# Optimization experiments

Hardware: AMD Instinct MI355X
Metric: run time of the kernel (lower is better)

Reference implementation:

```python
import jax, jax.numpy as jnp
import numpy as np

B, L, D = 16, 2048, 128
NEG = -1.0e9


def setup_inputs() -> dict:
    key = jax.random.key(0)
    kq, kk, kv, km = jax.random.split(key, 4)
    Q = jax.random.normal(kq, (B, L, D), dtype=jnp.float32)
    K = jax.random.normal(kk, (B, L, D), dtype=jnp.float32)
    V = jax.random.normal(kv, (B, L, D), dtype=jnp.float32)
    scale = jnp.float32(1.0 / np.sqrt(D))
    # original code masks rows where (mask + 1) == 0, i.e. mask == -1
    mask = jnp.where(jax.random.uniform(km, (B, L)) < 0.1, -1, 0).astype(jnp.int32)
    return {"Q": Q, "K": K, "V": V, "scale": scale, "mask": mask}


def reference(Q, K, V, scale, mask):
    # attention = Q @ K^T * scale  -> [B, Lq, Lk]
    att = jnp.einsum("bqd,bkd->bqk", Q, K) * scale
    # mask[b, i] broadcast over the key dim j (row-wise masking, as in the
    # original unsqueeze(-1).expand pattern with square attention)
    row_masked = (mask + 1) == 0  # [B, L]
    att = jnp.where(row_masked[:, :, None], NEG, att)
    att = jax.nn.softmax(att, axis=-1)
    context = jnp.einsum("bqk,bkd->bqd", att, V)
    return context
```

## Files before the change

### kernel.cpp

```cpp
#include <hip/hip_runtime.h>


#define NB 16
#define LL 2048
#define DD 128
#define LOG2E 1.44269504f
#define NM (-9.0f * 1.44269504f)

typedef __attribute__((ext_vector_type(8))) short short8;
typedef __attribute__((ext_vector_type(16))) float f32x16;

__device__ __forceinline__ float wexp2(float x) {
  float r; asm("v_exp_f32 %0, %1" : "=v"(r) : "v"(x)); return r;
}
__device__ __forceinline__ unsigned cvtpk(float lo, float hi) {
  unsigned r; asm("v_cvt_pk_bf16_f32 %0, %1, %2" : "=v"(r) : "v"(lo), "v"(hi)); return r;
}
__device__ __forceinline__ void gll16(const void* g, const void* l) {
  __builtin_amdgcn_global_load_lds(
      (const __attribute__((address_space(1))) unsigned*)g,
      (__attribute__((address_space(3))) unsigned*)l, 16, 0, 0);
}

__global__ void prep_kv(const float* __restrict__ K, const float* __restrict__ V,
                        short* __restrict__ Kb, short* __restrict__ Vt) {
  __shared__ short lds[64 * 130];
  int bid = blockIdx.x;
  int t = threadIdx.x;
  if (bid < 2048) {
    int g = bid * 256 + t;
    const float4* kp = (const float4*)K + (size_t)g * 2;
    float4 a = kp[0], c = kp[1];
    ((uint4*)Kb)[g] = make_uint4(cvtpk(a.x, a.y), cvtpk(a.z, a.w),
                                 cvtpk(c.x, c.y), cvtpk(c.z, c.w));
    return;
  }
  int vb = bid - 2048;
  int b = vb >> 5;
  int t0 = (vb & 31) * 64;
  #pragma unroll
  for (int i = 0; i < 8; ++i) {
    int c = t + i * 256;
    int kv = c >> 5, ds = (c & 31) * 4;
    float4 v = *(const float4*)(V + ((size_t)(b * LL + t0 + kv) * DD + ds));
    unsigned* dst = (unsigned*)(&lds[kv * 130 + ds]);
    dst[0] = cvtpk(v.x, v.y);
    dst[1] = cvtpk(v.z, v.w);
  }
  __syncthreads();
  int d = t >> 1, hf = t & 1;
  unsigned dw[16];
  #pragma unroll
  for (int i = 0; i < 16; ++i) {
    int kv = hf * 32 + i * 2;
    unsigned lo16 = (unsigned short)lds[kv * 130 + d];
    unsigned hi16 = (unsigned short)lds[(kv + 1) * 130 + d];
    dw[i] = lo16 | (hi16 << 16);
  }
  short* orow = Vt + (size_t)(b * DD + d) * LL + t0 + hf * 32;
  #pragma unroll
  for (int i = 0; i < 4; ++i)
    ((uint4*)orow)[i] = make_uint4(dw[4 * i], dw[4 * i + 1], dw[4 * i + 2], dw[4 * i + 3]);
}

__global__ __launch_bounds__(512, 2) void attn_main(
    const float* __restrict__ Q, const float* __restrict__ scl,
    const int* __restrict__ mask, const short* __restrict__ Kb,
    const short* __restrict__ Vt, float* __restrict__ Out) {
  __shared__ __align__(16) char smem[99840];
  const int tid = threadIdx.x;
  const int w = tid >> 6, l = tid & 63, lo = l & 31, hi = l >> 5;
  const int qg = w & 3, kvh = w >> 2;

  int lg = (blockIdx.x & 7) * 32 + (blockIdx.x >> 3);
  int b = lg >> 4;
  int q0 = (lg & 15) * 128 + qg * 32;

  int qrow = b * LL + q0 + lo;
  float msc = (mask[qrow] == -1) ? 0.f : scl[0];
  short8 qf[8];
  {
    const float* qp = Q + (size_t)qrow * DD + hi * 8;
    #pragma unroll
    for (int dc = 0; dc < 8; ++dc) {
      float4 a = *(const float4*)(qp + dc * 16);
      float4 c = *(const float4*)(qp + dc * 16 + 4);
      union { unsigned u[4]; short8 s; } pu;
      pu.u[0] = cvtpk(a.x * msc, a.y * msc);
      pu.u[1] = cvtpk(a.z * msc, a.w * msc);
      pu.u[2] = cvtpk(c.x * msc, c.y * msc);
      pu.u[3] = cvtpk(c.z * msc, c.w * msc);
      qf[dc] = pu.s;
    }
  }

  const char* kgb = (const char*)(Kb + (size_t)b * (LL * DD));
  const char* vgb = (const char*)(Vt + (size_t)b * (LL * DD));

#define STAGE(bi_, kv0_) do { \
    char* kbuf = smem + (bi_) * 16384; \
    char* vbuf = smem + 49152 + (bi_) * 16384; \
    _Pragma("unroll") \
    for (int i = 0; i < 2; ++i) { \
      int c = w * 2 + i; \
      int kr = c * 4 + (l >> 4); \
      int kc = ((l & 15) << 4) ^ ((kr & 15) << 4); \
      gll16(kgb + (size_t)((kv0_) + kr) * 256 + kc, kbuf + c * 1024); \
      int vr = c * 8 + (l >> 3); \
      int vc = ((l & 7) << 4) ^ ((vr & 7) << 4); \
      gll16(vgb + (size_t)vr * 4096 + (size_t)(kv0_) * 2 + vc, vbuf + c * 1024); \
    } \
  } while (0)

  STAGE(0, 0);
  STAGE(1, 64);

  f32x16 oacc[4];
  #pragma unroll
  for (int dt = 0; dt < 4; ++dt)
    #pragma unroll
    for (int r = 0; r < 16; ++r) oacc[dt][r] = 0.f;
  float lsum = 0.f;

  const int swzk = (lo & 15) << 4;
  const int swzv = (lo & 7) << 4;

  int cb = 0, sb = 2;
  #pragma unroll 1
  for (int t = 0; t < 32; ++t) {
    if (t == 31) { asm volatile("s_waitcnt vmcnt(0)" ::: "memory"); }
    else         { asm volatile("s_waitcnt vmcnt(4)" ::: "memory"); }
    __builtin_amdgcn_s_barrier();
    __builtin_amdgcn_sched_barrier(0);
    if (t < 30) STAGE(sb, (t + 2) * 64);

    const char* kb = smem + cb * 16384;
    const char* vb = smem + 49152 + cb * 16384;

    f32x16 acc;
    #pragma unroll
    for (int r = 0; r < 16; ++r) acc[r] = 0.f;
    const char* krow = kb + (kvh * 32 + lo) * 256;
    #pragma unroll
    for (int dc = 0; dc < 8; ++dc) {
      short8 kf = *(const short8*)(krow + ((dc * 32 + hi * 16) ^ swzk));
      acc = __builtin_amdgcn_mfma_f32_32x32x16_bf16(kf, qf[dc], acc, 0, 0, 0);
    }
    float ps = 0.f;
    #pragma unroll
    for (int r = 0; r < 16; ++r) {
      float p = wexp2(__builtin_fmaf(acc[r], LOG2E, NM));
      acc[r] = p; ps += p;
    }
    lsum += ps;
    short8 pa[2];
    #pragma unroll
    for (int ks = 0; ks < 2; ++ks) {
      unsigned a0 = cvtpk(acc[ks * 8 + 0], acc[ks * 8 + 1]);
      unsigned b0 = cvtpk(acc[ks * 8 + 4], acc[ks * 8 + 5]);
      unsigned c0 = cvtpk(acc[ks * 8 + 2], acc[ks * 8 + 3]);
      unsigned d0 = cvtpk(acc[ks * 8 + 6], acc[ks * 8 + 7]);
      asm volatile("v_permlane32_swap_b32 %0, %1" : "+v"(a0), "+v"(b0));
      asm volatile("v_permlane32_swap_b32 %0, %1" : "+v"(c0), "+v"(d0));
      union { unsigned u[4]; short8 s; } pu;
      pu.u[0] = a0; pu.u[1] = c0; pu.u[2] = b0; pu.u[3] = d0;
      pa[ks] = pu.s;
    }
    #pragma unroll
    for (int dt = 0; dt < 4; ++dt) {
      const char* vrow = vb + (dt * 32 + lo) * 128;
      #pragma unroll
      for (int ks = 0; ks < 2; ++ks) {
        short8 vf = *(const short8*)(vrow + ((kvh * 64 + ks * 32 + hi * 16) ^ swzv));
        oacc[dt] = __builtin_amdgcn_mfma_f32_32x32x16_bf16(pa[ks], vf, oacc[dt], 0, 0, 0);
      }
    }
    cb = (cb == 2) ? 0 : cb + 1;
    sb = (sb == 2) ? 0 : sb + 1;
  }
#undef STAGE

  float* lsb = (float*)(smem + 98304);
  float* rdb = (float*)(smem + 98304 + 1024);
  __syncthreads();
  if (kvh == 1) {
    char* reg = smem + qg * 16384;
    #pragma unroll
    for (int dt = 0; dt < 4; ++dt)
      #pragma unroll
      for (int i = 0; i < 4; ++i)
        *(float4*)(reg + l * 256 + ((dt * 64 + i * 16) ^ ((l & 15) << 4))) =
            make_float4(oacc[dt][4 * i], oacc[dt][4 * i + 1],
                        oacc[dt][4 * i + 2], oacc[dt][4 * i + 3]);
    lsb[qg * 64 + l] = lsum;
  }
  __syncthreads();
  if (kvh == 0) {
    char* reg = smem + qg * 16384;
    lsum += lsb[qg * 64 + l];
    #pragma unroll
    for (int dt = 0; dt < 4; ++dt)
      #pragma unroll
      for (int i = 0; i < 4; ++i) {
        float4 p = *(const float4*)(reg + l * 256 + ((dt * 64 + i * 16) ^ ((l & 15) << 4)));
        oacc[dt][4 * i + 0] += p.x;
        oacc[dt][4 * i + 1] += p.y;
        oacc[dt][4 * i + 2] += p.z;
        oacc[dt][4 * i + 3] += p.w;
      }
    float lt = lsum + __shfl_xor(lsum, 32);
    float rd = 1.0f / lt;
    if (l < 32) rdb[qg * 32 + l] = rd;
    #pragma unroll
    for (int r = 0; r < 16; ++r) {
      int cr = (r & 3) + 8 * (r >> 2) + 4 * hi;
      float rr = rdb[qg * 32 + cr];
      float* op = Out + (size_t)(b * LL + q0 + cr) * DD + lo;
      #pragma unroll
      for (int dt = 0; dt < 4; ++dt)
        op[dt * 32] = oacc[dt][r] * rr;
    }
  }
}

extern "C" void kernel_launch(void* const* d_in, const int* in_sizes, int n_in,
                              void* d_out, int out_size, void* d_ws, size_t ws_size,
                              hipStream_t stream) {
  const float* Q = (const float*)d_in[0];
  const float* K = (const float*)d_in[1];
  const float* V = (const float*)d_in[2];
  const float* scale = (const float*)d_in[3];
  const int* mask = (const int*)d_in[4];
  float* out = (float*)d_out;

  const size_t tensor_elems = (size_t)NB * LL * DD;
  const size_t need = 2 * tensor_elems * sizeof(short);
  if (ws_size < need) return;

  short* Kbp = (short*)d_ws;
  short* Vtp = Kbp + tensor_elems;

  hipLaunchKernelGGL(prep_kv, dim3(2560), dim3(256), 0, stream, K, V, Kbp, Vtp);
  hipLaunchKernelGGL(attn_main, dim3(256), dim3(512), 0, stream, Q, scale, mask, Kbp, Vtp, out);
}
```

Before: 60.67 us.

## Enlarge KV tile to 128 rows with double buffering in attention loop

The KV tile per iteration doubles to 128 rows and the pipeline goes from triple to double buffering, halving loop iterations and barriers. Each wave now computes two independent QK MFMA chains and feeds four P fragments into the PV MFMAs, which adds instruction-level parallelism. In exchange, shared memory use rises to about 130 KB, the prefetch depth shrinks to one tile with a full vmcnt(0) wait each iteration, and per-block occupancy may fall.

```diff
diff --git a/kernel.cpp b/kernel.cpp
--- a/kernel.cpp
+++ b/kernel.cpp
@@ -67,7 +67,7 @@
     const float* __restrict__ Q, const float* __restrict__ scl,
     const int* __restrict__ mask, const short* __restrict__ Kb,
     const short* __restrict__ Vt, float* __restrict__ Out) {
-  __shared__ __align__(16) char smem[99840];
+  __shared__ __align__(16) char smem[132608];
   const int tid = threadIdx.x;
   const int w = tid >> 6, l = tid & 63, lo = l & 31, hi = l >> 5;
   const int qg = w & 3, kvh = w >> 2;
@@ -75,6 +75,24 @@
   int lg = (blockIdx.x & 7) * 32 + (blockIdx.x >> 3);
   int b = lg >> 4;
   int q0 = (lg & 15) * 128 + qg * 32;
+
+  const char* kgb = (const char*)(Kb + (size_t)b * (LL * DD));
+  const char* vgb = (const char*)(Vt + (size_t)b * (LL * DD));
+
+#define STAGE(bi_, kv0_) do { \
+    char* kbuf = smem + (bi_) * 32768; \
+    char* vbuf = smem + 65536 + (bi_) * 32768; \
+    _Pragma("unroll") \
+    for (int i = 0; i < 4; ++i) { \
+      int c = tid + i * 512; \
+      int kr = c >> 4; \
+      int kc = ((c & 15) << 4) ^ ((kr & 15) << 4); \
+      gll16(kgb + (size_t)((kv0_) + kr) * 256 + kc, kbuf + c * 16); \
+      gll16(vgb + (size_t)kr * 4096 + (size_t)(kv0_) * 2 + kc, vbuf + c * 16); \
+    } \
+  } while (0)
+
+  STAGE(0, 0);
 
   int qrow = b * LL + q0 + lo;
   float msc = (mask[qrow] == -1) ? 0.f : scl[0];
@@ -94,27 +112,6 @@
     }
   }
 
-  const char* kgb = (const char*)(Kb + (size_t)b * (LL * DD));
-  const char* vgb = (const char*)(Vt + (size_t)b * (LL * DD));
-
-#define STAGE(bi_, kv0_) do { \
-    char* kbuf = smem + (bi_) * 16384; \
-    char* vbuf = smem + 49152 + (bi_) * 16384; \
-    _Pragma("unroll") \
-    for (int i = 0; i < 2; ++i) { \
-      int c = w * 2 + i; \
-      int kr = c * 4 + (l >> 4); \
-      int kc = ((l & 15) << 4) ^ ((kr & 15) << 4); \
-      gll16(kgb + (size_t)((kv0_) + kr) * 256 + kc, kbuf + c * 1024); \
-      int vr = c * 8 + (l >> 3); \
-      int vc = ((l & 7) << 4) ^ ((vr & 7) << 4); \
-      gll16(vgb + (size_t)vr * 4096 + (size_t)(kv0_) * 2 + vc, vbuf + c * 1024); \
-    } \
-  } while (0)
-
-  STAGE(0, 0);
-  STAGE(1, 64);
-
   f32x16 oacc[4];
   #pragma unroll
   for (int dt = 0; dt < 4; ++dt)
@@ -122,66 +119,72 @@
     for (int r = 0; r < 16; ++r) oacc[dt][r] = 0.f;
   float lsum = 0.f;
 
-  const int swzk = (lo & 15) << 4;
-  const int swzv = (lo & 7) << 4;
-
-  int cb = 0, sb = 2;
+  const int swz = (lo & 15) << 4;
+
+  int cur = 0;
   #pragma unroll 1
-  for (int t = 0; t < 32; ++t) {
-    if (t == 31) { asm volatile("s_waitcnt vmcnt(0)" ::: "memory"); }
-    else         { asm volatile("s_waitcnt vmcnt(4)" ::: "memory"); }
+  for (int t = 0; t < 16; ++t) {
+    asm volatile("s_waitcnt vmcnt(0)" ::: "memory");
     __builtin_amdgcn_s_barrier();
     __builtin_amdgcn_sched_barrier(0);
-    if (t < 30) STAGE(sb, (t + 2) * 64);
-
-    const char* kb = smem + cb * 16384;
-    const char* vb = smem + 49152 + cb * 16384;
-
-    f32x16 acc;
-    #pragma unroll
-    for (int r = 0; r < 16; ++r) acc[r] = 0.f;
-    const char* krow = kb + (kvh * 32 + lo) * 256;
+    if (t < 15) STAGE(cur ^ 1, (t + 1) * 128);
+
+    const char* kb = smem + cur * 32768;
+    const char* vb = smem + 65536 + cur * 32768;
+
+    f32x16 accA, accB;
+    #pragma unroll
+    for (int r = 0; r < 16; ++r) { accA[r] = 0.f; accB[r] = 0.f; }
+    const char* krow0 = kb + (kvh * 64 + lo) * 256;
+    const char* krow1 = kb + (kvh * 64 + 32 + lo) * 256;
     #pragma unroll
     for (int dc = 0; dc < 8; ++dc) {
-      short8 kf = *(const short8*)(krow + ((dc * 32 + hi * 16) ^ swzk));
-      acc = __builtin_amdgcn_mfma_f32_32x32x16_bf16(kf, qf[dc], acc, 0, 0, 0);
+      int kcol = (dc * 32 + hi * 16) ^ swz;
+      short8 kfA = *(const short8*)(krow0 + kcol);
+      short8 kfB = *(const short8*)(krow1 + kcol);
+      accA = __builtin_amdgcn_mfma_f32_32x32x16_bf16(kfA, qf[dc], accA, 0, 0, 0);
+      accB = __builtin_amdgcn_mfma_f32_32x32x16_bf16(kfB, qf[dc], accB, 0, 0, 0);
     }
     float ps = 0.f;
     #pragma unroll
     for (int r = 0; r < 16; ++r) {
-      float p = wexp2(__builtin_fmaf(acc[r], LOG2E, NM));
-      acc[r] = p; ps += p;
+      float pA = wexp2(__builtin_fmaf(accA[r], LOG2E, NM));
+      float pB = wexp2(__builtin_fmaf(accB[r], LOG2E, NM));
+      accA[r] = pA; accB[r] = pB; ps += pA + pB;
     }
     lsum += ps;
-    short8 pa[2];
-    #pragma unroll
-    for (int ks = 0; ks < 2; ++ks) {
-      unsigned a0 = cvtpk(acc[ks * 8 + 0], acc[ks * 8 + 1]);
-      unsigned b0 = cvtpk(acc[ks * 8 + 4], acc[ks * 8 + 5]);
-      unsigned c0 = cvtpk(acc[ks * 8 + 2], acc[ks * 8 + 3]);
-      unsigned d0 = cvtpk(acc[ks * 8 + 6], acc[ks * 8 + 7]);
-      asm volatile("v_permlane32_swap_b32 %0, %1" : "+v"(a0), "+v"(b0));
-      asm volatile("v_permlane32_swap_b32 %0, %1" : "+v"(c0), "+v"(d0));
-      union { unsigned u[4]; short8 s; } pu;
-      pu.u[0] = a0; pu.u[1] = c0; pu.u[2] = b0; pu.u[3] = d0;
-      pa[ks] = pu.s;
+    short8 pa[4];
+    #pragma unroll
+    for (int bk = 0; bk < 2; ++bk) {
+      const f32x16& ac = bk ? accB : accA;
+      #pragma unroll
+      for (int ks = 0; ks < 2; ++ks) {
+        unsigned a0 = cvtpk(ac[ks * 8 + 0], ac[ks * 8 + 1]);
+        unsigned b0 = cvtpk(ac[ks * 8 + 4], ac[ks * 8 + 5]);
+        unsigned c0 = cvtpk(ac[ks * 8 + 2], ac[ks * 8 + 3]);
+        unsigned d0 = cvtpk(ac[ks * 8 + 6], ac[ks * 8 + 7]);
+        asm volatile("v_permlane32_swap_b32 %0, %1" : "+v"(a0), "+v"(b0));
+        asm volatile("v_permlane32_swap_b32 %0, %1" : "+v"(c0), "+v"(d0));
+        union { unsigned u[4]; short8 s; } pu;
+        pu.u[0] = a0; pu.u[1] = c0; pu.u[2] = b0; pu.u[3] = d0;
+        pa[bk * 2 + ks] = pu.s;
+      }
     }
     #pragma unroll
     for (int dt = 0; dt < 4; ++dt) {
-      const char* vrow = vb + (dt * 32 + lo) * 128;
-      #pragma unroll
-      for (int ks = 0; ks < 2; ++ks) {
-        short8 vf = *(const short8*)(vrow + ((kvh * 64 + ks * 32 + hi * 16) ^ swzv));
-        oacc[dt] = __builtin_amdgcn_mfma_f32_32x32x16_bf16(pa[ks], vf, oacc[dt], 0, 0, 0);
+      const char* vrow = vb + (dt * 32 + lo) * 256;
+      #pragma unroll
+      for (int j = 0; j < 4; ++j) {
+        short8 vf = *(const short8*)(vrow + ((kvh * 128 + j * 32 + hi * 16) ^ swz));
+        oacc[dt] = __builtin_amdgcn_mfma_f32_32x32x16_bf16(pa[j], vf, oacc[dt], 0, 0, 0);
       }
     }
-    cb = (cb == 2) ? 0 : cb + 1;
-    sb = (sb == 2) ? 0 : sb + 1;
+    cur ^= 1;
   }
 #undef STAGE
 
-  float* lsb = (float*)(smem + 98304);
-  float* rdb = (float*)(smem + 98304 + 1024);
+  float* lsb = (float*)(smem + 131072);
+  float* rdb = (float*)(smem + 132096);
   __syncthreads();
   if (kvh == 1) {
     char* reg = smem + qg * 16384;
```

Result: no change. 59.48 us (-2.0%).
